# Kernel tuning notes

Hardware: AMD Instinct MI355X
Metric: run time of the kernel (lower is better)

The kernel has to match this reference:

```python
import jax, jax.numpy as jnp
import numpy as np

B, T, N, F_IN = 8, 12, 20000, 2
H, HORIZON, K = 64, 12, 2
E = 320000


def setup_inputs() -> dict:
    key = jax.random.key(0)
    ks = jax.random.split(key, 12)
    s = 0.05
    return dict(
        x=jax.random.normal(ks[0], (B, T, N, F_IN), jnp.float32),
        edge_index=jax.random.randint(ks[1], (2, E), 0, N),
        edge_weight=jax.random.uniform(ks[2], (E,), jnp.float32),
        enc_w=jax.random.normal(ks[3], (F_IN, H), jnp.float32) * s,
        enc_b=jnp.zeros((H,), jnp.float32),
        node_emb=jax.random.normal(ks[4], (N, H), jnp.float32) * s,
        w_ih=jax.random.normal(ks[5], (3 * H, H), jnp.float32) * s,
        w_hh=jax.random.normal(ks[6], (3 * H, H), jnp.float32) * s,
        b_ih=jnp.zeros((3 * H,), jnp.float32),
        b_hh=jnp.zeros((3 * H,), jnp.float32),
        filt_w=jax.random.normal(ks[7], (H * (2 * K + 1), H), jnp.float32) * s,
        filt_b=jnp.zeros((H,), jnp.float32),
        dec_w=jax.random.normal(ks[8], (H, F_IN * HORIZON), jnp.float32) * s,
        dec_b=jnp.zeros((F_IN * HORIZON,), jnp.float32),
    )


def _gru_last(x_seq, w_ih, w_hh, b_ih, b_hh):
    # x_seq: [BN, T, H] -> last hidden state [BN, H] (torch GRU gate math)
    bn = x_seq.shape[0]
    h0 = jnp.zeros((bn, H), x_seq.dtype)
    # precompute input-side gates: [T, BN, 3H]
    xg = jnp.swapaxes(jnp.einsum('bth,gh->btg', x_seq, w_ih) + b_ih, 0, 1)

    def step(h, xg_t):
        hg = h @ w_hh.T + b_hh
        xr, xz, xn = jnp.split(xg_t, 3, axis=-1)
        hr, hz, hn = jnp.split(hg, 3, axis=-1)
        r = jax.nn.sigmoid(xr + hr)
        z = jax.nn.sigmoid(xz + hz)
        n = jnp.tanh(xn + r * hn)
        return (1.0 - z) * n + z * h, None

    h_last, _ = jax.lax.scan(step, h0, xg)
    return h_last


def _norm_weights(w, idx):
    # normalize edge weights by in-degree of aggregation index (tsl normalize)
    deg = jax.ops.segment_sum(w, idx, num_segments=N)
    inv = jnp.where(deg > 0, 1.0 / deg, 0.0)
    return w * inv[idx]


def _propagate(h, src, tgt, w):
    # h: [B, N, H]; message x_j * w aggregated (sum) at target
    msg = h[:, src, :] * w[None, :, None]           # [B, E, H]
    return jnp.zeros_like(h).at[:, tgt, :].add(msg)


def reference(x, edge_index, edge_weight, enc_w, enc_b, node_emb,
              w_ih, w_hh, b_ih, b_hh, filt_w, filt_b, dec_w, dec_b):
    b, t, n, _ = x.shape
    # linear encode + node embeddings
    x_emb = x @ enc_w + enc_b + node_emb[None, None]          # [B, T, N, H]
    # per-node GRU over time
    x_rnn = jnp.transpose(x_emb, (0, 2, 1, 3)).reshape(b * n, t, H)
    h = _gru_last(x_rnn, w_ih, w_hh, b_ih, b_hh).reshape(b, n, H)
    # diffusion graph conv: root + k hops forward + k hops backward
    src, tgt = edge_index[0], edge_index[1]
    w_fwd = _norm_weights(edge_weight, tgt)
    w_bwd = _norm_weights(edge_weight, src)
    outs = [h]
    for s_idx, t_idx, w in ((src, tgt, w_fwd), (tgt, src, w_bwd)):
        hs = h
        for _ in range(K):
            hs = _propagate(hs, s_idx, t_idx, w)
            outs.append(hs)
    z = jnp.concatenate(outs, axis=-1) @ filt_w + filt_b      # [B, N, H]
    # decode and rearrange 'b n (t f) -> b t n f'
    x_out = z @ dec_w + dec_b                                 # [B, N, HORIZON*F_IN]
    x_hor = x_out.reshape(b, n, HORIZON, F_IN)
    return jnp.transpose(x_hor, (0, 2, 1, 3))                 # [B, HORIZON, N, F_IN]
```

## Files before the change

### kernel.cpp

```cpp
#include <hip/hip_runtime.h>

#define NN 20000
#define NE 320000
#define NB 8
#define NT 12

typedef unsigned int u32;
typedef short bf16x8 __attribute__((ext_vector_type(8)));
typedef float f32x4 __attribute__((ext_vector_type(4)));

union U8 { u32 u[4]; bf16x8 v; };

__device__ __forceinline__ float bcast(float v, int k) {
  return __int_as_float(__builtin_amdgcn_readlane(__float_as_int(v), k));
}
__device__ __forceinline__ u32 cvt_pk_bf16(float a, float b) {
  u32 r;
  asm("v_cvt_pk_bf16_f32 %0, %1, %2" : "=v"(r) : "v"(a), "v"(b));
  return r;
}
__device__ __forceinline__ float rcpf(float x) {
  float r;
  asm("v_rcp_f32 %0, %1" : "=v"(r) : "v"(x));
  return r;
}
__device__ __forceinline__ unsigned short f2bf(float f) {
  u32 u = __float_as_uint(f);
  u32 r = (u + 0x7FFFu + ((u >> 16) & 1u)) >> 16;
  return (unsigned short)r;
}
__device__ __forceinline__ float bf2f(unsigned short s) {
  return __uint_as_float(((u32)s) << 16);
}

__global__ void deg_kernel(const int* __restrict__ ei, const float* __restrict__ ew,
                           float* __restrict__ wsum_f, float* __restrict__ wsum_b,
                           int* __restrict__ cnt_f, int* __restrict__ cnt_b) {
  int e = blockIdx.x * 256 + threadIdx.x;
  if (e >= NE) return;
  int s = ei[e], t = ei[NE + e];
  float wv = ew[e];
  atomicAdd(&wsum_f[t], wv);
  atomicAdd(&cnt_f[t], 1);
  atomicAdd(&wsum_b[s], wv);
  atomicAdd(&cnt_b[s], 1);
}

__global__ __launch_bounds__(1024) void scan_kernel(
    const int* __restrict__ cnt_f, const int* __restrict__ cnt_b,
    int* __restrict__ rp_f, int* __restrict__ rp_b,
    int* __restrict__ cur_f, int* __restrict__ cur_b) {
  __shared__ int sm[1024];
  const int tid = threadIdx.x;
  for (int pass = 0; pass < 2; ++pass) {
    const int* cnt = pass ? cnt_b : cnt_f;
    int* rp  = pass ? rp_b  : rp_f;
    int* cur = pass ? cur_b : cur_f;
    const int base = tid * 20;
    int4 c4[5];
    int s = 0;
    if (base < NN) {
      const int4* cp = (const int4*)(cnt + base);
#pragma unroll
      for (int j = 0; j < 5; j++) c4[j] = cp[j];
#pragma unroll
      for (int j = 0; j < 5; j++) s += c4[j].x + c4[j].y + c4[j].z + c4[j].w;
    }
    __syncthreads();
    sm[tid] = s;
    __syncthreads();
    for (int off = 1; off < 1024; off <<= 1) {
      int v = (tid >= off) ? sm[tid - off] : 0;
      __syncthreads();
      sm[tid] += v;
      __syncthreads();
    }
    if (base < NN) {
      int run = sm[tid] - s;
      int4* rp4  = (int4*)(rp + base);
      int4* cur4 = (int4*)(cur + base);
#pragma unroll
      for (int j = 0; j < 5; j++) {
        int4 o;
        o.x = run; run += c4[j].x;
        o.y = run; run += c4[j].y;
        o.z = run; run += c4[j].z;
        o.w = run; run += c4[j].w;
        rp4[j] = o;
        cur4[j] = o;
      }
    }
    if (tid == 1023) rp[NN] = sm[1023];
  }
}

__global__ void fill_kernel(const int* __restrict__ ei, const float* __restrict__ ew,
                            const float* __restrict__ wsum_f, const float* __restrict__ wsum_b,
                            int* __restrict__ cur_f, int* __restrict__ cur_b,
                            int* __restrict__ col_f, float* __restrict__ wn_f,
                            int* __restrict__ col_b, float* __restrict__ wn_b) {
  int e = blockIdx.x * 256 + threadIdx.x;
  if (e >= NE) return;
  int s = ei[e], t = ei[NE + e];
  float wv = ew[e];
  int slot = atomicAdd(&cur_f[t], 1);
  float w1 = wsum_f[t];
  col_f[slot] = s;
  wn_f[slot] = (w1 > 0.f) ? wv / w1 : 0.f;
  slot = atomicAdd(&cur_b[s], 1);
  float w2 = wsum_b[s];
  col_b[slot] = t;
  wn_b[slot] = (w2 > 0.f) ? wv / w2 : 0.f;
}

#define NBLK_NB 313
__global__ __launch_bounds__(512) void nb_kernel(
    const float* __restrict__ node_emb, const float* __restrict__ enc_b,
    const float* __restrict__ w_ih, const float* __restrict__ b_ih,
    const float* __restrict__ enc_w, const float* __restrict__ b_hh,
    const float* __restrict__ filt_w, const float* __restrict__ filt_b,
    const float* __restrict__ dec_w, const float* __restrict__ dec_b,
    float* __restrict__ nbq, float* __restrict__ W2,
    float* __restrict__ Wcat, float* __restrict__ cbv) {
  const int tid = threadIdx.x;
  if (blockIdx.x >= NBLK_NB) {
    int idx = (blockIdx.x - NBLK_NB) * 512 + tid;
    if (idx < 64 * 128) {
      int k = idx >> 7, j = idx & 127;
      float acc = 0.f;
      if (j < 120) {
        int wi = j / 24, jj = j - wi * 24;
        for (int c = 0; c < 64; c++)
          acc += filt_w[(wi * 64 + k) * 64 + c] * dec_w[c * 24 + jj];
      }
      Wcat[idx] = acc;
    } else if (idx < 64 * 128 + 24) {
      int jj = idx - 64 * 128;
      float acc = dec_b[jj];
      for (int c = 0; c < 64; c++) acc += filt_b[c] * dec_w[c * 24 + jj];
      cbv[jj] = acc;
    }
    return;
  }
  __shared__ float w3[64 * 64 * 4];
  for (int idx = tid; idx < 192 * 64; idx += 512) {
    int row = idx >> 6, k = idx & 63;
    w3[((k << 6) + (row & 63)) * 4 + (row >> 6)] = w_ih[idx];
  }
  __syncthreads();
  const int lane = tid & 63, wave = tid >> 6;
  const float4* w3v = (const float4*)w3;
  const float eb = enc_b[lane];
  const float bir = b_ih[lane], biz = b_ih[64 + lane], bin_ = b_ih[128 + lane];
  const float bhr = b_hh[lane], bhz = b_hh[64 + lane];
#pragma unroll 1
  for (int pass = 0; pass < 8; ++pass) {
    const int n = blockIdx.x * 64 + pass * 8 + wave;
    if (n >= NN) break;
    float ne = node_emb[n * 64 + lane] + eb;
    float ar = bir, az = biz, an = bin_;
#pragma unroll 16
    for (int k = 0; k < 64; k++) {
      float4 w = w3v[(k << 6) + lane];
      float nk = bcast(ne, k);
      ar = fmaf(w.x, nk, ar);
      az = fmaf(w.y, nk, az);
      an = fmaf(w.z, nk, an);
    }
    nbq[(((lane >> 2)) * NN + n) * 4 + (lane & 3)]      = ar + bhr;
    nbq[((16 + (lane >> 2)) * NN + n) * 4 + (lane & 3)] = az + bhz;
    nbq[((32 + (lane >> 2)) * NN + n) * 4 + (lane & 3)] = an;
  }
  if (blockIdx.x == 0 && tid < 384) {
    int f = tid / 192, g = tid - f * 192;
    float acc = 0.f;
    for (int k2 = 0; k2 < 64; k2++) acc += enc_w[f * 64 + k2] * w_ih[g * 64 + k2];
    W2[f * 192 + g] = acc;
  }
}

#define MFMA(acc, a, b) acc = __builtin_amdgcn_mfma_f32_16x16x32_bf16((a), (b), acc, 0, 0, 0)
#define BP(addr, reg) __builtin_amdgcn_ds_bpermute((addr), (int)(reg))

__global__ __launch_bounds__(256, 3) void gru_kernel(
    const float* __restrict__ x, const float* __restrict__ nbq,
    const float* __restrict__ W2, const float* __restrict__ b_hh,
    const float* __restrict__ w_hh, const float* __restrict__ Wcat,
    const float* __restrict__ cbv,
    float* __restrict__ G0, float* __restrict__ G1f, float* __restrict__ G2f,
    float* __restrict__ G1b, float* __restrict__ G2b) {
  __shared__ u32 lds[12288];
  const int tid = threadIdx.x;

  for (int idx = tid; idx < 6144; idx += 256) {
    int tile = idx >> 9, ks = (idx >> 8) & 1, ln = (idx >> 2) & 63, r = idx & 3;
    int gate = tile * 16 + (ln & 15);
    int k2 = ks * 32 + ((ln >> 4) & 3) * 8 + r * 2;
    float w0 = w_hh[gate * 64 + k2];
    float w1 = w_hh[gate * 64 + k2 + 1];
    unsigned short h0 = f2bf(w0), h1 = f2bf(w1);
    unsigned short l0 = f2bf(w0 - bf2f(h0)), l1 = f2bf(w1 - bf2f(h1));
    lds[idx]        = (u32)h0 | ((u32)h1 << 16);
    lds[6144 + idx] = (u32)l0 | ((u32)l1 << 16);
  }
  __syncthreads();

  const int lane = tid & 63, wave = tid >> 6;
  const int g = lane >> 4, sl = lane & 15;
  const int seq = blockIdx.x * 64 + wave * 16 + sl;
  const int bb = seq / NN;
  const int node = seq - bb * NN;
  const int addrA = (((g & 1) * 32) + sl) * 4;
  const int addrB = addrA + 64;
  const bool fbHi = (g >= 2);

#define LDW(tile, ks, part) (*(const bf16x8*)(lds + (part) * 6144 + (((tile) * 2 + (ks)) << 8) + (lane << 2)))

#define BLD(hb, lb, fo) { \
    int a_, b_; \
    a_ = BP(addrA, hiP[fo]); b_ = BP(addrA, hiP[(fo) + 1]); hb.u[0] = fbHi ? b_ : a_; \
    a_ = BP(addrA, hiQ[fo]); b_ = BP(addrA, hiQ[(fo) + 1]); hb.u[1] = fbHi ? b_ : a_; \
    a_ = BP(addrB, hiP[fo]); b_ = BP(addrB, hiP[(fo) + 1]); hb.u[2] = fbHi ? b_ : a_; \
    a_ = BP(addrB, hiQ[fo]); b_ = BP(addrB, hiQ[(fo) + 1]); hb.u[3] = fbHi ? b_ : a_; \
    a_ = BP(addrA, loP[fo]); b_ = BP(addrA, loP[(fo) + 1]); lb.u[0] = fbHi ? b_ : a_; \
    a_ = BP(addrA, loQ[fo]); b_ = BP(addrA, loQ[(fo) + 1]); lb.u[1] = fbHi ? b_ : a_; \
    a_ = BP(addrB, loP[fo]); b_ = BP(addrB, loP[(fo) + 1]); lb.u[2] = fbHi ? b_ : a_; \
    a_ = BP(addrB, loQ[fo]); b_ = BP(addrB, loQ[(fo) + 1]); lb.u[3] = fbHi ? b_ : a_; \
  }

  u32 w2h[12], w2l[12];
#pragma unroll
  for (int tl = 0; tl < 12; tl++) {
    float w0 = W2[tl * 16 + sl], w1 = W2[192 + tl * 16 + sl];
    u32 ph = cvt_pk_bf16(w0, w1);
    float lo0 = w0 - __uint_as_float(ph << 16);
    float lo1 = w1 - __uint_as_float(ph & 0xffff0000u);
    u32 pl = cvt_pk_bf16(lo0, lo1);
    w2h[tl] = (lane < 16) ? ph : 0u;
    w2l[tl] = (lane < 16) ? pl : 0u;
  }

  f32x4 nbA[4], nbB[4], nbC[4], bhnv[4];
#pragma unroll
  for (int fb = 0; fb < 4; fb++) {
    nbA[fb]  = *(const f32x4*)(nbq + ((size_t)(fb * 4 + g) * NN + node) * 4);
    nbB[fb]  = *(const f32x4*)(nbq + ((size_t)(16 + fb * 4 + g) * NN + node) * 4);
    nbC[fb]  = *(const f32x4*)(nbq + ((size_t)(32 + fb * 4 + g) * NN + node) * 4);
    bhnv[fb] = *(const f32x4*)(b_hh + 128 + fb * 16 + g * 4);
  }

  f32x4 hreg[4];
#pragma unroll
  for (int fb = 0; fb < 4; fb++) hreg[fb] = (f32x4){0.f, 0.f, 0.f, 0.f};

  u32 hiP[4], hiQ[4], loP[4], loQ[4];

  const float* xptr = x + ((size_t)(bb * NT) * NN + node) * 2;

  U8 hb0, hb1, lb0, lb1;

  float2 xv = *(const float2*)(xptr);

#pragma unroll 1
  for (int t = 0; t < NT; t++) {
    float2 xvn;
    if (t + 1 < NT) xvn = *(const float2*)(xptr + (size_t)(t + 1) * (NN * 2));
    u32 xhw = cvt_pk_bf16(xv.x, xv.y);
    float xl0 = xv.x - __uint_as_float(xhw << 16);
    float xl1 = xv.y - __uint_as_float(xhw & 0xffff0000u);
    u32 xlw = cvt_pk_bf16(xl0, xl1);
    U8 xB;
    xB.u[0] = xhw; xB.u[1] = xlw; xB.u[2] = xhw; xB.u[3] = 0u;

    if (t) { BLD(hb0, lb0, 0); BLD(hb1, lb1, 2); }

#pragma unroll
    for (int fb = 0; fb < 4; fb++) {
      f32x4 aR = nbA[fb], aZ = nbB[fb], aXN = nbC[fb], aHN = bhnv[fb];
      if (t) {
        bf16x8 Ah0 = LDW(fb, 0, 0), Al0 = LDW(fb, 0, 1);
        bf16x8 Ah1 = LDW(fb, 1, 0), Al1 = LDW(fb, 1, 1);
        MFMA(aR, Ah0, hb0.v); MFMA(aR, Ah0, lb0.v); MFMA(aR, Al0, hb0.v);
        MFMA(aR, Ah1, hb1.v); MFMA(aR, Ah1, lb1.v); MFMA(aR, Al1, hb1.v);
        bf16x8 Bh0 = LDW(4 + fb, 0, 0), Bl0 = LDW(4 + fb, 0, 1);
        bf16x8 Bh1 = LDW(4 + fb, 1, 0), Bl1 = LDW(4 + fb, 1, 1);
        MFMA(aZ, Bh0, hb0.v); MFMA(aZ, Bh0, lb0.v); MFMA(aZ, Bl0, hb0.v);
        MFMA(aZ, Bh1, hb1.v); MFMA(aZ, Bh1, lb1.v); MFMA(aZ, Bl1, hb1.v);
        bf16x8 Ch0 = LDW(8 + fb, 0, 0), Cl0 = LDW(8 + fb, 0, 1);
        bf16x8 Ch1 = LDW(8 + fb, 1, 0), Cl1 = LDW(8 + fb, 1, 1);
        MFMA(aHN, Ch0, hb0.v); MFMA(aHN, Ch0, lb0.v); MFMA(aHN, Cl0, hb0.v);
        MFMA(aHN, Ch1, hb1.v); MFMA(aHN, Ch1, lb1.v); MFMA(aHN, Cl1, hb1.v);
      }
      U8 aW;
      aW.u[0] = w2h[fb];     aW.u[1] = w2h[fb];     aW.u[2] = w2l[fb];     aW.u[3] = 0u;
      MFMA(aR, aW.v, xB.v);
      aW.u[0] = w2h[4 + fb]; aW.u[1] = w2h[4 + fb]; aW.u[2] = w2l[4 + fb];
      MFMA(aZ, aW.v, xB.v);
      aW.u[0] = w2h[8 + fb]; aW.u[1] = w2h[8 + fb]; aW.u[2] = w2l[8 + fb];
      MFMA(aXN, aW.v, xB.v);

      float hv[4];
#pragma unroll
      for (int r = 0; r < 4; r++) {
        float rr = rcpf(1.f + __expf(-aR[r]));
        float zz = rcpf(1.f + __expf(-aZ[r]));
        float nv = fmaf(rr, aHN[r], aXN[r]);
        float th = fmaf(-2.f, rcpf(1.f + __expf(2.f * nv)), 1.f);
        float h2 = fmaf(zz, hreg[fb][r] - th, th);
        hreg[fb][r] = h2;
        hv[r] = h2;
      }
      u32 hA = cvt_pk_bf16(hv[0], hv[1]);
      u32 hB = cvt_pk_bf16(hv[2], hv[3]);
      float l0 = hv[0] - __uint_as_float(hA << 16);
      float l1 = hv[1] - __uint_as_float(hA & 0xffff0000u);
      float l2 = hv[2] - __uint_as_float(hB << 16);
      float l3 = hv[3] - __uint_as_float(hB & 0xffff0000u);
      hiP[fb] = hA;
      hiQ[fb] = hB;
      loP[fb] = cvt_pk_bf16(l0, l1);
      loQ[fb] = cvt_pk_bf16(l2, l3);
    }
    xv = xvn;
  }

  __syncthreads();
  for (int idx = tid; idx < 4096; idx += 256) {
    int tile = idx >> 9, ks = (idx >> 8) & 1, ln = (idx >> 2) & 63, r = idx & 3;
    int j = tile * 16 + (ln & 15);
    int k2 = ks * 32 + ((ln >> 4) & 3) * 8 + r * 2;
    float w0 = Wcat[k2 * 128 + j];
    float w1 = Wcat[(k2 + 1) * 128 + j];
    unsigned short h0 = f2bf(w0), h1 = f2bf(w1);
    unsigned short l0 = f2bf(w0 - bf2f(h0)), l1 = f2bf(w1 - bf2f(h1));
    lds[idx]        = (u32)h0 | ((u32)h1 << 16);
    lds[4096 + idx] = (u32)l0 | ((u32)l1 << 16);
  }
  __syncthreads();
  BLD(hb0, lb0, 0); BLD(hb1, lb1, 2);

#define LDC(tile, ks, part) (*(const bf16x8*)(lds + (part) * 4096 + (((tile) * 2 + (ks)) << 8) + (lane << 2)))
#pragma unroll
  for (int tile = 0; tile < 8; tile++) {
    f32x4 acc = (f32x4){0.f, 0.f, 0.f, 0.f};
    bf16x8 Ah0 = LDC(tile, 0, 0), Al0 = LDC(tile, 0, 1);
    MFMA(acc, Ah0, hb0.v); MFMA(acc, Ah0, lb0.v); MFMA(acc, Al0, hb0.v);
    bf16x8 Ah1 = LDC(tile, 1, 0), Al1 = LDC(tile, 1, 1);
    MFMA(acc, Ah1, hb1.v); MFMA(acc, Ah1, lb1.v); MFMA(acc, Al1, hb1.v);
#pragma unroll
    for (int r = 0; r < 4; r++) {
      int j = tile * 16 + g * 4 + r;
      if (j < 120) {
        int wi = j / 24, jj = j - wi * 24;
        float val = acc[r];
        if (wi == 0) val += cbv[jj];
        float* gb = (wi == 0) ? G0 : (wi == 1) ? G1f : (wi == 2) ? G2f : (wi == 3) ? G1b : G2b;
        gb[((size_t)node * NB + bb) * 24 + jj] = val;
      }
    }
  }
}

__global__ __launch_bounds__(256) void hop1_kernel(
    float* __restrict__ G1f, const float* __restrict__ G2f,
    float* __restrict__ G1b, const float* __restrict__ G2b,
    const int* __restrict__ rp_f, const int* __restrict__ col_f, const float* __restrict__ wn_f,
    const int* __restrict__ rp_b, const int* __restrict__ col_b, const float* __restrict__ wn_b) {
  const int wv = threadIdx.x >> 6;
  const int lane = threadIdx.x & 63;
  const int task = blockIdx.x * 4 + wv;
  const int fwd = task < NN;
  const int n = fwd ? task : task - NN;
  const int* rp  = fwd ? rp_f : rp_b;
  const int* col = fwd ? col_f : col_b;
  const float* wn = fwd ? wn_f : wn_b;
  const float4* src = (const float4*)(fwd ? G2f : G2b);
  float4* dst = (float4*)(fwd ? G1f : G1b);
  const int e0 = rp[n], e1 = rp[n + 1];
  if (lane >= 48) return;
  float4 acc0 = {0.f, 0.f, 0.f, 0.f};
  float4 acc1 = {0.f, 0.f, 0.f, 0.f};
  int e = e0;
  for (; e + 1 < e1; e += 2) {
    const int c0 = col[e], c1 = col[e + 1];
    const float w0 = wn[e], w1 = wn[e + 1];
    float4 v0 = src[(size_t)c0 * 48 + lane];
    float4 v1 = src[(size_t)c1 * 48 + lane];
    acc0.x = fmaf(w0, v0.x, acc0.x); acc1.x = fmaf(w1, v1.x, acc1.x);
    acc0.y = fmaf(w0, v0.y, acc0.y); acc1.y = fmaf(w1, v1.y, acc1.y);
    acc0.z = fmaf(w0, v0.z, acc0.z); acc1.z = fmaf(w1, v1.z, acc1.z);
    acc0.w = fmaf(w0, v0.w, acc0.w); acc1.w = fmaf(w1, v1.w, acc1.w);
  }
  if (e < e1) {
    const int c0 = col[e];
    const float w0 = wn[e];
    float4 v0 = src[(size_t)c0 * 48 + lane];
    acc0.x = fmaf(w0, v0.x, acc0.x);
    acc0.y = fmaf(w0, v0.y, acc0.y);
    acc0.z = fmaf(w0, v0.z, acc0.z);
    acc0.w = fmaf(w0, v0.w, acc0.w);
  }
  float4 d = dst[(size_t)n * 48 + lane];
  d.x += acc0.x + acc1.x;
  d.y += acc0.y + acc1.y;
  d.z += acc0.z + acc1.z;
  d.w += acc0.w + acc1.w;
  dst[(size_t)n * 48 + lane] = d;
}

__global__ __launch_bounds__(256) void hop2_kernel(
    float* __restrict__ G0, const float* __restrict__ G1f, const float* __restrict__ G1b,
    const int* __restrict__ rp_f, const int* __restrict__ col_f, const float* __restrict__ wn_f,
    const int* __restrict__ rp_b, const int* __restrict__ col_b, const float* __restrict__ wn_b) {
  const int wv = threadIdx.x >> 6;
  const int lane = threadIdx.x & 63;
  const int n = blockIdx.x * 4 + wv;
  if (lane >= 48) return;
  const float4* s1 = (const float4*)G1f;
  const float4* s2 = (const float4*)G1b;
  float4* dst = (float4*)G0;
  float4 acc0 = dst[(size_t)n * 48 + lane];
  float4 acc1 = {0.f, 0.f, 0.f, 0.f};
#pragma unroll 1
  for (int pass = 0; pass < 2; ++pass) {
    const int* rp  = pass ? rp_b : rp_f;
    const int* col = pass ? col_b : col_f;
    const float* wn = pass ? wn_b : wn_f;
    const float4* src = pass ? s2 : s1;
    const int e0 = rp[n], e1 = rp[n + 1];
    int e = e0;
    for (; e + 1 < e1; e += 2) {
      const int c0 = col[e], c1 = col[e + 1];
      const float w0 = wn[e], w1 = wn[e + 1];
      float4 v0 = src[(size_t)c0 * 48 + lane];
      float4 v1 = src[(size_t)c1 * 48 + lane];
      acc0.x = fmaf(w0, v0.x, acc0.x); acc1.x = fmaf(w1, v1.x, acc1.x);
      acc0.y = fmaf(w0, v0.y, acc0.y); acc1.y = fmaf(w1, v1.y, acc1.y);
      acc0.z = fmaf(w0, v0.z, acc0.z); acc1.z = fmaf(w1, v1.z, acc1.z);
      acc0.w = fmaf(w0, v0.w, acc0.w); acc1.w = fmaf(w1, v1.w, acc1.w);
    }
    if (e < e1) {
      const int c0 = col[e];
      const float w0 = wn[e];
      float4 v0 = src[(size_t)c0 * 48 + lane];
      acc0.x = fmaf(w0, v0.x, acc0.x);
      acc0.y = fmaf(w0, v0.y, acc0.y);
      acc0.z = fmaf(w0, v0.z, acc0.z);
      acc0.w = fmaf(w0, v0.w, acc0.w);
    }
  }
  acc0.x += acc1.x; acc0.y += acc1.y; acc0.z += acc1.z; acc0.w += acc1.w;
  dst[(size_t)n * 48 + lane] = acc0;
}

__global__ __launch_bounds__(256) void reorder_kernel(const float* __restrict__ G0,
                                                      float* __restrict__ out) {
  __shared__ float tile[32 * 193];
  const int n0 = blockIdx.x * 32;
  const int tid = threadIdx.x;
  for (int idx = tid; idx < 6144; idx += 256) {
    int i = idx / 192, r = idx - i * 192;
    tile[i * 193 + r] = G0[(size_t)n0 * 192 + idx];
  }
  __syncthreads();
  for (int idx = tid; idx < 6144; idx += 256) {
    int b = idx / 768;
    int rem = idx - b * 768;
    int t = rem >> 6;
    int rem2 = rem & 63;
    int i = rem2 >> 1, f = rem2 & 1;
    out[(((size_t)b * NT + t) * NN + n0 + i) * 2 + f] = tile[i * 193 + b * 24 + t * 2 + f];
  }
}

extern "C" void kernel_launch(void* const* d_in, const int* in_sizes, int n_in,
                              void* d_out, int out_size, void* d_ws, size_t ws_size,
                              hipStream_t stream) {
  const float* x        = (const float*)d_in[0];
  const int*   ei       = (const int*)d_in[1];
  const float* ew       = (const float*)d_in[2];
  const float* enc_w    = (const float*)d_in[3];
  const float* enc_b    = (const float*)d_in[4];
  const float* node_emb = (const float*)d_in[5];
  const float* w_ih     = (const float*)d_in[6];
  const float* w_hh     = (const float*)d_in[7];
  const float* b_ih     = (const float*)d_in[8];
  const float* b_hh     = (const float*)d_in[9];
  const float* filt_w   = (const float*)d_in[10];
  const float* filt_b   = (const float*)d_in[11];
  const float* dec_w    = (const float*)d_in[12];
  const float* dec_b    = (const float*)d_in[13];
  float* out = (float*)d_out;

  char* p = (char*)d_ws;
  auto alloc = [&](size_t bytes) {
    char* r = p;
    p += (bytes + 255) & ~(size_t)255;
    return r;
  };
  const size_t BN24 = (size_t)NB * NN * 24;
  float* G0   = (float*)alloc(BN24 * 4);
  float* G1f  = (float*)alloc(BN24 * 4);
  float* G2f  = (float*)alloc(BN24 * 4);
  float* G1b  = (float*)alloc(BN24 * 4);
  float* G2b  = (float*)alloc(BN24 * 4);
  float* nbq  = (float*)alloc((size_t)NN * 192 * 4);
  int* rp_f   = (int*)alloc((NN + 1) * 4);
  int* rp_b   = (int*)alloc((NN + 1) * 4);
  char* zreg  = alloc(4 * NN * 4);
  float* wsum_f = (float*)zreg;
  float* wsum_b = wsum_f + NN;
  int*   cnt_f  = (int*)(wsum_b + NN);
  int*   cnt_b  = cnt_f + NN;
  int* cur_f  = (int*)alloc(NN * 4);
  int* cur_b  = (int*)alloc(NN * 4);
  int* col_f  = (int*)alloc((size_t)NE * 4);
  float* wn_f = (float*)alloc((size_t)NE * 4);
  int* col_b  = (int*)alloc((size_t)NE * 4);
  float* wn_b = (float*)alloc((size_t)NE * 4);
  float* Wcat = (float*)alloc(64 * 128 * 4);
  float* cbv  = (float*)alloc(32 * 4);
  float* W2   = (float*)alloc(384 * 4);

  hipMemsetAsync(zreg, 0, 4 * NN * 4, stream);
  deg_kernel<<<(NE + 255) / 256, 256, 0, stream>>>(ei, ew, wsum_f, wsum_b, cnt_f, cnt_b);
  scan_kernel<<<1, 1024, 0, stream>>>(cnt_f, cnt_b, rp_f, rp_b, cur_f, cur_b);
  fill_kernel<<<(NE + 255) / 256, 256, 0, stream>>>(ei, ew, wsum_f, wsum_b, cur_f, cur_b,
                                                    col_f, wn_f, col_b, wn_b);
  nb_kernel<<<NBLK_NB + 17, 512, 0, stream>>>(node_emb, enc_b, w_ih, b_ih, enc_w, b_hh,
                                              filt_w, filt_b, dec_w, dec_b,
                                              nbq, W2, Wcat, cbv);
  gru_kernel<<<(NB * NN) / 64, 256, 0, stream>>>(x, nbq, W2, b_hh, w_hh, Wcat, cbv,
                                                 G0, G1f, G2f, G1b, G2b);
  hop1_kernel<<<2 * NN / 4, 256, 0, stream>>>(G1f, G2f, G1b, G2b,
                                              rp_f, col_f, wn_f, rp_b, col_b, wn_b);
  hop2_kernel<<<NN / 4, 256, 0, stream>>>(G0, G1f, G1b,
                                          rp_f, col_f, wn_f, rp_b, col_b, wn_b);
  reorder_kernel<<<NN / 32, 256, 0, stream>>>(G0, out);
}
```

Measured before the change: 558.6 us.

## Move low-bf16 weight halves to global memory and fuse output reorder into hop2

A new prep kernel precomputes the low-part bf16 splits of w_hh and the filter weights into global buffers. The GRU kernel now keeps only the high parts in LDS, halving LDS use to raise occupancy, and reads the low parts straight from global or cache inside the recurrent loop. Separately, hop2 writes its results directly in the final [B,T,N,F] layout, which removes the reorder kernel and one full G0 round trip. The cost is more global loads per MFMA step and uncoalesced float2 stores in hop2.

```diff
diff --git a/kernel.cpp b/kernel.cpp
--- a/kernel.cpp
+++ b/kernel.cpp
@@ -179,6 +179,30 @@
   }
 }
 
+__global__ __launch_bounds__(256) void prep_kernel(
+    const float* __restrict__ w_hh, const float* __restrict__ Wcat,
+    u32* __restrict__ whhLo, u32* __restrict__ wcatLo) {
+  int idx = blockIdx.x * 256 + threadIdx.x;
+  if (idx < 6144) {
+    int tile = idx >> 9, ks = (idx >> 8) & 1, ln = (idx >> 2) & 63, r = idx & 3;
+    int gate = tile * 16 + (ln & 15);
+    int k2 = ks * 32 + ((ln >> 4) & 3) * 8 + r * 2;
+    float w0 = w_hh[gate * 64 + k2];
+    float w1 = w_hh[gate * 64 + k2 + 1];
+    unsigned short h0 = f2bf(w0), h1 = f2bf(w1);
+    whhLo[idx] = (u32)f2bf(w0 - bf2f(h0)) | ((u32)f2bf(w1 - bf2f(h1)) << 16);
+  } else if (idx < 6144 + 4096) {
+    int e = idx - 6144;
+    int tile = e >> 9, ks = (e >> 8) & 1, ln = (e >> 2) & 63, r = e & 3;
+    int j = tile * 16 + (ln & 15);
+    int k2 = ks * 32 + ((ln >> 4) & 3) * 8 + r * 2;
+    float w0 = Wcat[k2 * 128 + j];
+    float w1 = Wcat[(k2 + 1) * 128 + j];
+    unsigned short h0 = f2bf(w0), h1 = f2bf(w1);
+    wcatLo[e] = (u32)f2bf(w0 - bf2f(h0)) | ((u32)f2bf(w1 - bf2f(h1)) << 16);
+  }
+}
+
 #define MFMA(acc, a, b) acc = __builtin_amdgcn_mfma_f32_16x16x32_bf16((a), (b), acc, 0, 0, 0)
 #define BP(addr, reg) __builtin_amdgcn_ds_bpermute((addr), (int)(reg))
 
@@ -186,10 +210,11 @@
     const float* __restrict__ x, const float* __restrict__ nbq,
     const float* __restrict__ W2, const float* __restrict__ b_hh,
     const float* __restrict__ w_hh, const float* __restrict__ Wcat,
+    const u32* __restrict__ whhLo, const u32* __restrict__ wcatLo,
     const float* __restrict__ cbv,
     float* __restrict__ G0, float* __restrict__ G1f, float* __restrict__ G2f,
     float* __restrict__ G1b, float* __restrict__ G2b) {
-  __shared__ u32 lds[12288];
+  __shared__ u32 lds[6144];
   const int tid = threadIdx.x;
 
   for (int idx = tid; idx < 6144; idx += 256) {
@@ -198,10 +223,7 @@
     int k2 = ks * 32 + ((ln >> 4) & 3) * 8 + r * 2;
     float w0 = w_hh[gate * 64 + k2];
     float w1 = w_hh[gate * 64 + k2 + 1];
-    unsigned short h0 = f2bf(w0), h1 = f2bf(w1);
-    unsigned short l0 = f2bf(w0 - bf2f(h0)), l1 = f2bf(w1 - bf2f(h1));
-    lds[idx]        = (u32)h0 | ((u32)h1 << 16);
-    lds[6144 + idx] = (u32)l0 | ((u32)l1 << 16);
+    lds[idx] = (u32)f2bf(w0) | ((u32)f2bf(w1) << 16);
   }
   __syncthreads();
 
@@ -214,7 +236,8 @@
   const int addrB = addrA + 64;
   const bool fbHi = (g >= 2);
 
-#define LDW(tile, ks, part) (*(const bf16x8*)(lds + (part) * 6144 + (((tile) * 2 + (ks)) << 8) + (lane << 2)))
+#define LDH(tile, ks) (*(const bf16x8*)(lds + (((tile) * 2 + (ks)) << 8) + (lane << 2)))
+#define LDL(tile, ks) (*(const bf16x8*)(whhLo + (((tile) * 2 + (ks)) << 8) + (lane << 2)))
 
 #define BLD(hb, lb, fo) { \
     int a_, b_; \
@@ -278,16 +301,16 @@
     for (int fb = 0; fb < 4; fb++) {
       f32x4 aR = nbA[fb], aZ = nbB[fb], aXN = nbC[fb], aHN = bhnv[fb];
       if (t) {
-        bf16x8 Ah0 = LDW(fb, 0, 0), Al0 = LDW(fb, 0, 1);
-        bf16x8 Ah1 = LDW(fb, 1, 0), Al1 = LDW(fb, 1, 1);
+        bf16x8 Ah0 = LDH(fb, 0), Al0 = LDL(fb, 0);
+        bf16x8 Ah1 = LDH(fb, 1), Al1 = LDL(fb, 1);
         MFMA(aR, Ah0, hb0.v); MFMA(aR, Ah0, lb0.v); MFMA(aR, Al0, hb0.v);
         MFMA(aR, Ah1, hb1.v); MFMA(aR, Ah1, lb1.v); MFMA(aR, Al1, hb1.v);
-        bf16x8 Bh0 = LDW(4 + fb, 0, 0), Bl0 = LDW(4 + fb, 0, 1);
-        bf16x8 Bh1 = LDW(4 + fb, 1, 0), Bl1 = LDW(4 + fb, 1, 1);
+        bf16x8 Bh0 = LDH(4 + fb, 0), Bl0 = LDL(4 + fb, 0);
+        bf16x8 Bh1 = LDH(4 + fb, 1), Bl1 = LDL(4 + fb, 1);
         MFMA(aZ, Bh0, hb0.v); MFMA(aZ, Bh0, lb0.v); MFMA(aZ, Bl0, hb0.v);
         MFMA(aZ, Bh1, hb1.v); MFMA(aZ, Bh1, lb1.v); MFMA(aZ, Bl1, hb1.v);
-        bf16x8 Ch0 = LDW(8 + fb, 0, 0), Cl0 = LDW(8 + fb, 0, 1);
-        bf16x8 Ch1 = LDW(8 + fb, 1, 0), Cl1 = LDW(8 + fb, 1, 1);
+        bf16x8 Ch0 = LDH(8 + fb, 0), Cl0 = LDL(8 + fb, 0);
+        bf16x8 Ch1 = LDH(8 + fb, 1), Cl1 = LDL(8 + fb, 1);
         MFMA(aHN, Ch0, hb0.v); MFMA(aHN, Ch0, lb0.v); MFMA(aHN, Cl0, hb0.v);
         MFMA(aHN, Ch1, hb1.v); MFMA(aHN, Ch1, lb1.v); MFMA(aHN, Cl1, hb1.v);
       }
@@ -331,21 +354,19 @@
     int k2 = ks * 32 + ((ln >> 4) & 3) * 8 + r * 2;
     float w0 = Wcat[k2 * 128 + j];
     float w1 = Wcat[(k2 + 1) * 128 + j];
-    unsigned short h0 = f2bf(w0), h1 = f2bf(w1);
-    unsigned short l0 = f2bf(w0 - bf2f(h0)), l1 = f2bf(w1 - bf2f(h1));
-    lds[idx]        = (u32)h0 | ((u32)h1 << 16);
-    lds[4096 + idx] = (u32)l0 | ((u32)l1 << 16);
+    lds[idx] = (u32)f2bf(w0) | ((u32)f2bf(w1) << 16);
   }
   __syncthreads();
   BLD(hb0, lb0, 0); BLD(hb1, lb1, 2);
 
-#define LDC(tile, ks, part) (*(const bf16x8*)(lds + (part) * 4096 + (((tile) * 2 + (ks)) << 8) + (lane << 2)))
+#define LCH(tile, ks) (*(const bf16x8*)(lds + (((tile) * 2 + (ks)) << 8) + (lane << 2)))
+#define LCL(tile, ks) (*(const bf16x8*)(wcatLo + (((tile) * 2 + (ks)) << 8) + (lane << 2)))
 #pragma unroll
   for (int tile = 0; tile < 8; tile++) {
     f32x4 acc = (f32x4){0.f, 0.f, 0.f, 0.f};
-    bf16x8 Ah0 = LDC(tile, 0, 0), Al0 = LDC(tile, 0, 1);
+    bf16x8 Ah0 = LCH(tile, 0), Al0 = LCL(tile, 0);
     MFMA(acc, Ah0, hb0.v); MFMA(acc, Ah0, lb0.v); MFMA(acc, Al0, hb0.v);
-    bf16x8 Ah1 = LDC(tile, 1, 0), Al1 = LDC(tile, 1, 1);
+    bf16x8 Ah1 = LCH(tile, 1), Al1 = LCL(tile, 1);
     MFMA(acc, Ah1, hb1.v); MFMA(acc, Ah1, lb1.v); MFMA(acc, Al1, hb1.v);
 #pragma unroll
     for (int r = 0; r < 4; r++) {
@@ -409,17 +430,17 @@
 }
 
 __global__ __launch_bounds__(256) void hop2_kernel(
-    float* __restrict__ G0, const float* __restrict__ G1f, const float* __restrict__ G1b,
+    const float* __restrict__ G0, const float* __restrict__ G1f, const float* __restrict__ G1b,
     const int* __restrict__ rp_f, const int* __restrict__ col_f, const float* __restrict__ wn_f,
-    const int* __restrict__ rp_b, const int* __restrict__ col_b, const float* __restrict__ wn_b) {
+    const int* __restrict__ rp_b, const int* __restrict__ col_b, const float* __restrict__ wn_b,
+    float* __restrict__ out) {
   const int wv = threadIdx.x >> 6;
   const int lane = threadIdx.x & 63;
   const int n = blockIdx.x * 4 + wv;
   if (lane >= 48) return;
   const float4* s1 = (const float4*)G1f;
   const float4* s2 = (const float4*)G1b;
-  float4* dst = (float4*)G0;
-  float4 acc0 = dst[(size_t)n * 48 + lane];
+  float4 acc0 = ((const float4*)G0)[(size_t)n * 48 + lane];
   float4 acc1 = {0.f, 0.f, 0.f, 0.f};
 #pragma unroll 1
   for (int pass = 0; pass < 2; ++pass) {
@@ -450,27 +471,13 @@
     }
   }
   acc0.x += acc1.x; acc0.y += acc1.y; acc0.z += acc1.z; acc0.w += acc1.w;
-  dst[(size_t)n * 48 + lane] = acc0;
-}
-
-__global__ __launch_bounds__(256) void reorder_kernel(const float* __restrict__ G0,
-                                                      float* __restrict__ out) {
-  __shared__ float tile[32 * 193];
-  const int n0 = blockIdx.x * 32;
-  const int tid = threadIdx.x;
-  for (int idx = tid; idx < 6144; idx += 256) {
-    int i = idx / 192, r = idx - i * 192;
-    tile[i * 193 + r] = G0[(size_t)n0 * 192 + idx];
-  }
-  __syncthreads();
-  for (int idx = tid; idx < 6144; idx += 256) {
-    int b = idx / 768;
-    int rem = idx - b * 768;
-    int t = rem >> 6;
-    int rem2 = rem & 63;
-    int i = rem2 >> 1, f = rem2 & 1;
-    out[(((size_t)b * NT + t) * NN + n0 + i) * 2 + f] = tile[i * 193 + b * 24 + t * 2 + f];
-  }
+  const int b = lane / 6;
+  const int jj0 = (lane - b * 6) * 4;
+  const int t0 = jj0 >> 1;
+  float2* o0 = (float2*)(out + (((size_t)b * NT + t0) * NN + n) * 2);
+  float2* o1 = (float2*)(out + (((size_t)b * NT + t0 + 1) * NN + n) * 2);
+  *o0 = (float2){acc0.x, acc0.y};
+  *o1 = (float2){acc0.z, acc0.w};
 }
 
 extern "C" void kernel_launch(void* const* d_in, const int* in_sizes, int n_in,
@@ -521,6 +528,8 @@
   float* Wcat = (float*)alloc(64 * 128 * 4);
   float* cbv  = (float*)alloc(32 * 4);
   float* W2   = (float*)alloc(384 * 4);
+  u32* whhLo  = (u32*)alloc(6144 * 4);
+  u32* wcatLo = (u32*)alloc(4096 * 4);
 
   hipMemsetAsync(zreg, 0, 4 * NN * 4, stream);
   deg_kernel<<<(NE + 255) / 256, 256, 0, stream>>>(ei, ew, wsum_f, wsum_b, cnt_f, cnt_b);
@@ -530,11 +539,12 @@
   nb_kernel<<<NBLK_NB + 17, 512, 0, stream>>>(node_emb, enc_b, w_ih, b_ih, enc_w, b_hh,
                                               filt_w, filt_b, dec_w, dec_b,
                                               nbq, W2, Wcat, cbv);
-  gru_kernel<<<(NB * NN) / 64, 256, 0, stream>>>(x, nbq, W2, b_hh, w_hh, Wcat, cbv,
+  prep_kernel<<<40, 256, 0, stream>>>(w_hh, Wcat, whhLo, wcatLo);
+  gru_kernel<<<(NB * NN) / 64, 256, 0, stream>>>(x, nbq, W2, b_hh, w_hh, Wcat,
+                                                 whhLo, wcatLo, cbv,
                                                  G0, G1f, G2f, G1b, G2b);
   hop1_kernel<<<2 * NN / 4, 256, 0, stream>>>(G1f, G2f, G1b, G2b,
                                               rp_f, col_f, wn_f, rp_b, col_b, wn_b);
   hop2_kernel<<<NN / 4, 256, 0, stream>>>(G0, G1f, G1b,
-                                          rp_f, col_f, wn_f, rp_b, col_b, wn_b);
-  reorder_kernel<<<NN / 32, 256, 0, stream>>>(G0, out);
-}
+                                          rp_f, col_f, wn_f, rp_b, col_b, wn_b, out);
+}
```

After: 874.1 us. 56.5% more time.
